# Optimization experiments

Measured on AMD Instinct MI355X. Metric: run time of the kernel, lower is better.

The kernel has to match this reference:

```python
import jax, jax.numpy as jnp
import numpy as np

B, D, S, L = 4, 512, 2048, 8921

def setup_inputs() -> dict:
    key = jax.random.key(0)
    ks = jax.random.split(key, 4)
    H = jax.random.normal(ks[0], (B, D, S), dtype=jnp.float32)
    # 1x1 conv weights collapse to [out, in] matrices (xavier-ish scale)
    Wk = jax.random.normal(ks[1], (D, D), dtype=jnp.float32) * (1.0 / np.sqrt(D))
    Wv = jax.random.normal(ks[2], (D, D), dtype=jnp.float32) * (1.0 / np.sqrt(D))
    bk = jnp.full((D,), 0.01, dtype=jnp.float32)
    bv = jnp.full((D,), 0.01, dtype=jnp.float32)
    Q = jax.random.normal(ks[3], (L, D), dtype=jnp.float32) * 0.02
    return {"H": H, "Wk": Wk, "bk": bk, "Wv": Wv, "bv": bv, "Q": Q}

def reference(H, Wk, bk, Wv, bv, Q):
    # K/V: 1x1 Conv1d over channels + bias, ELU, permute(0,2,1) -> [B,S,D]
    K = jax.nn.elu(jnp.einsum('od,bds->bso', Wk, H) + bk)
    V = jax.nn.elu(jnp.einsum('od,bds->bso', Wv, H) + bv)
    # TargetAttention: energy E = Q K^T -> [B,L,S], softmax over seq (scale=False)
    E = jnp.einsum('ld,bsd->bls', Q, K)
    A = jax.nn.softmax(E, axis=-1)
    C = jnp.einsum('bls,bsd->bld', A, V)  # [B, L, D]
    return (C, A)
```

## Files before the change

kernel.cpp:

```cpp
#include <hip/hip_runtime.h>
#include <math.h>

#define Bn 4
#define Dn 512
#define Sn 2048
#define Ln 8921
#define Lpad 8960

typedef short bf16x8 __attribute__((ext_vector_type(8)));
typedef float f32x4 __attribute__((ext_vector_type(4)));

__device__ __forceinline__ float elu1(float x) {
    return x > 0.f ? x : expm1f(x);
}

__device__ __forceinline__ unsigned f2bf(float f) {
    unsigned u = __float_as_uint(f);
    u += 0x7FFFu + ((u >> 16) & 1u);
    return u >> 16;
}
__device__ __forceinline__ unsigned pack2(float a, float b) {
    return f2bf(a) | (f2bf(b) << 16);
}
__device__ __forceinline__ unsigned pack_bf_trunc(float lo, float hi) {
    return __builtin_amdgcn_perm(__float_as_uint(hi), __float_as_uint(lo), 0x07060302u);
}
__device__ __forceinline__ void gld_lds16(const void* g, void* l) {
    __builtin_amdgcn_global_load_lds((const __attribute__((address_space(1))) int*)g,
                                     (__attribute__((address_space(3))) int*)l, 16, 0, 0);
}

__global__ __launch_bounds__(256) void h_transpose(const float* __restrict__ H,
                                                   short* __restrict__ Ht) {
    int b = blockIdx.z;
    int s0 = blockIdx.x * 64, d0 = blockIdx.y * 64;
    __shared__ float tile[64][65];
    int t = threadIdx.x;
    int r = t >> 4, c4 = (t & 15) * 4;
    const float* Hb = H + (size_t)b * Dn * Sn;
#pragma unroll
    for (int i = 0; i < 4; ++i) {
        float4 v = *(const float4*)(Hb + (size_t)(d0 + i * 16 + r) * Sn + s0 + c4);
        *(float4*)&tile[i * 16 + r][c4] = v;
    }
    __syncthreads();
#pragma unroll
    for (int i = 0; i < 4; ++i) {
        int srow = i * 16 + r;
        float v0 = tile[c4 + 0][srow], v1 = tile[c4 + 1][srow];
        float v2 = tile[c4 + 2][srow], v3 = tile[c4 + 3][srow];
        uint2 o = make_uint2(pack2(v0, v1), pack2(v2, v3));
        *(uint2*)(Ht + ((size_t)b * Sn + s0 + srow) * Dn + d0 + c4) = o;
    }
}

__global__ __launch_bounds__(256) void f32_to_bf16(const float* __restrict__ src,
                                                   short* __restrict__ dst, int n8) {
    int id = blockIdx.x * 256 + threadIdx.x;
    if (id >= n8) return;
    const float* s = src + (size_t)id * 8;
    float4 a = *(const float4*)s;
    float4 b = *(const float4*)(s + 4);
    uint4 o = {pack2(a.x, a.y), pack2(a.z, a.w), pack2(b.x, b.y), pack2(b.z, b.w)};
    *(uint4*)(dst + (size_t)id * 8) = o;
}

__global__ __launch_bounds__(256) void q_to_bf16(const float* __restrict__ Q,
                                                 short* __restrict__ Qb) {
    int id = blockIdx.x * 256 + threadIdx.x;
    int row = id >> 6, c = (id & 63) * 8;
    uint4 o = {0, 0, 0, 0};
    if (row < Ln) {
        const float* src = Q + (size_t)row * Dn + c;
        float4 a = *(const float4*)src;
        float4 b = *(const float4*)(src + 4);
        o.x = pack2(a.x, a.y); o.y = pack2(a.z, a.w);
        o.z = pack2(b.x, b.y); o.w = pack2(b.z, b.w);
    }
    *(uint4*)(Qb + (size_t)id * 8) = o;
}

template <int OUT_BF16, int EPI>
__global__ __launch_bounds__(256) void gemm_nt(const short* __restrict__ A,
                                               const short* __restrict__ B,
                                               const float* __restrict__ bias,
                                               void* __restrict__ Out,
                                               int K, int lda, int ldb, int ldo,
                                               int mmax,
                                               long bA, long bB, long bO) {
    const int b  = blockIdx.z;
    const int n0 = blockIdx.x * 128;
    const int m0 = blockIdx.y * 128;
    __shared__ short lA[128 * 32];
    __shared__ short lB[128 * 32];
    const int t = threadIdx.x;
    const int lane = t & 63, w = t >> 6;
    const int wm = (w & 1) * 64, wn = (w >> 1) * 64;
    const int quad = lane >> 4, l15 = lane & 15;
    f32x4 acc[4][4] = {};
    const short* Ab = A + (size_t)bA * b + (size_t)m0 * lda;
    const short* Bb = B + (size_t)bB * b + (size_t)n0 * ldb;
    const int sr = t >> 2, ss = (t & 3) * 8;

    for (int k0 = 0; k0 < K; k0 += 32) {
        gld_lds16(Ab + (size_t)sr * lda + k0 + ss,        lA + t * 8);
        gld_lds16(Ab + (size_t)(sr + 64) * lda + k0 + ss, lA + 2048 + t * 8);
        gld_lds16(Bb + (size_t)sr * ldb + k0 + ss,        lB + t * 8);
        gld_lds16(Bb + (size_t)(sr + 64) * ldb + k0 + ss, lB + 2048 + t * 8);
        __syncthreads();
        bf16x8 af[4], bfr[4];
#pragma unroll
        for (int i = 0; i < 4; ++i)
            af[i] = *(const bf16x8*)&lA[(wm + i * 16 + l15) * 32 + quad * 8];
#pragma unroll
        for (int j = 0; j < 4; ++j)
            bfr[j] = *(const bf16x8*)&lB[(wn + j * 16 + l15) * 32 + quad * 8];
#pragma unroll
        for (int i = 0; i < 4; ++i)
#pragma unroll
            for (int j = 0; j < 4; ++j)
                acc[i][j] = __builtin_amdgcn_mfma_f32_16x16x32_bf16(af[i], bfr[j], acc[i][j], 0, 0, 0);
        __syncthreads();
    }

#pragma unroll
    for (int i = 0; i < 4; ++i) {
        int mb = m0 + wm + i * 16 + quad * 4;
#pragma unroll
        for (int r = 0; r < 4; ++r) {
            int m = mb + r;
            if (m < mmax) {
                float bm = (EPI == 2) ? bias[m] : 0.f;
#pragma unroll
                for (int j = 0; j < 4; ++j) {
                    int col = n0 + wn + j * 16 + l15;
                    float v = acc[i][j][r];
                    if (EPI == 1) v = elu1(v + bias[col]);
                    if (EPI == 2) v = elu1(v + bm);
                    if (OUT_BF16)
                        ((short*)Out)[(size_t)bO * b + (size_t)m * ldo + col] = (short)f2bf(v);
                    else
                        ((float*)Out)[(size_t)bO * b + (size_t)m * ldo + col] = v;
                }
            }
        }
    }
}

template <int OUT_BF16, int BN>
__global__ __launch_bounds__(512, 2) void gemm_ntp(const short* __restrict__ A,
                                                   const short* __restrict__ B,
                                                   void* __restrict__ Out,
                                                   int K, int lda, int ldb, int ldo,
                                                   int mmax,
                                                   long bA, long bB, long bO) {
    constexpr int NWN   = BN / 64;
    constexpr int WSPAN = 32 * NWN;
    constexpr int WMF   = 2 * NWN;
    constexpr int BCH   = BN * 4;
    constexpr int SLOT  = 8192 + BN * 32;
    constexpr int TPB   = 2 + BN / 128;
    __shared__ short lds[4 * SLOT];

    int GX = gridDim.x, GY = gridDim.y;
    int nwg = GX * GY * gridDim.z;
    int lin = blockIdx.x + GX * (blockIdx.y + GY * blockIdx.z);
    int wid = lin;
    if ((nwg & 7) == 0) wid = (lin & 7) * (nwg >> 3) + (lin >> 3);
    int bx = wid % GX; wid /= GX;
    int by = wid % GY;
    int bz = wid / GY;

    const int b  = bz;
    const int n0 = bx * BN;
    const int m0 = by * 256;
    const int t = threadIdx.x;
    const int lane = t & 63, w = t >> 6;
    const int wn = w % NWN, wm = w / NWN;
    const int quad = lane >> 4, l15 = lane & 15;
    const int xr = (l15 >> 1) & 3;

    const short* Ab = A + (size_t)bA * b + (size_t)m0 * lda;
    const short* Bb = B + (size_t)bB * b + (size_t)n0 * ldb;

    const short* srcA[2]; int dstA[2];
#pragma unroll
    for (int i = 0; i < 2; ++i) {
        int p = i * 512 + t;
        int g = p ^ ((p >> 3) & 3);
        srcA[i] = Ab + (size_t)(g >> 2) * lda + (g & 3) * 8;
        dstA[i] = p * 8;
    }
    const short* srcB[2]; int dstB[2];
#pragma unroll
    for (int i = 0; i < BCH / 512; ++i) {
        int p = i * 512 + t;
        int g = p ^ ((p >> 3) & 3);
        srcB[i] = Bb + (size_t)(g >> 2) * ldb + (g & 3) * 8;
        dstB[i] = 8192 + p * 8;
    }

    int offA[WMF], offB[4];
#pragma unroll
    for (int m = 0; m < WMF; ++m) {
        int c = (wm * WSPAN + m * 16 + l15) * 4 + quad;
        offA[m] = (c ^ xr) * 8;
    }
#pragma unroll
    for (int j = 0; j < 4; ++j) {
        int c = (wn * 64 + j * 16 + l15) * 4 + quad;
        offB[j] = 8192 + (c ^ xr) * 8;
    }

    f32x4 acc[WMF][4] = {};
    const int NK = K >> 5;

    auto STAGE_A = [&](int kt) {
        const int slot = (kt & 3) * SLOT;
        const int ko = kt * 32;
        gld_lds16(srcA[0] + ko, &lds[slot + dstA[0]]);
        gld_lds16(srcA[1] + ko, &lds[slot + dstA[1]]);
    };
    auto STAGE_B = [&](int kt) {
        const int slot = (kt & 3) * SLOT;
        const int ko = kt * 32;
        gld_lds16(srcB[0] + ko, &lds[slot + dstB[0]]);
        if constexpr (BN == 256) gld_lds16(srcB[1] + ko, &lds[slot + dstB[1]]);
    };

    STAGE_A(0); STAGE_B(0);
    STAGE_A(1); STAGE_B(1);
    STAGE_A(2); STAGE_B(2);

    for (int k = 0; k < NK; ++k) {
        asm volatile("s_waitcnt lgkmcnt(0)" ::: "memory");
        if constexpr (TPB == 4) {
            if (k < NK - 2)       asm volatile("s_waitcnt vmcnt(8)" ::: "memory");
            else if (k == NK - 2) asm volatile("s_waitcnt vmcnt(4)" ::: "memory");
            else                  asm volatile("s_waitcnt vmcnt(0)" ::: "memory");
        } else {
            if (k < NK - 2)       asm volatile("s_waitcnt vmcnt(6)" ::: "memory");
            else if (k == NK - 2) asm volatile("s_waitcnt vmcnt(3)" ::: "memory");
            else                  asm volatile("s_waitcnt vmcnt(0)" ::: "memory");
        }
        __builtin_amdgcn_s_barrier();
        asm volatile("" ::: "memory");
        const short* sl = &lds[(k & 3) * SLOT];

        bf16x8 af[WMF], bfv[4];
#pragma unroll
        for (int j = 0; j < 4; ++j) bfv[j] = *(const bf16x8*)(sl + offB[j]);
#pragma unroll
        for (int m = 0; m < WMF / 2; ++m) af[m] = *(const bf16x8*)(sl + offA[m]);
        if (k + 3 < NK) STAGE_A(k + 3);
        asm volatile("s_waitcnt lgkmcnt(0)" ::: "memory");
        __builtin_amdgcn_s_barrier();
        __builtin_amdgcn_s_setprio(1);
#pragma unroll
        for (int m = 0; m < WMF / 2; ++m)
#pragma unroll
            for (int j = 0; j < 4; ++j)
                acc[m][j] = __builtin_amdgcn_mfma_f32_16x16x32_bf16(af[m], bfv[j], acc[m][j], 0, 0, 0);
        __builtin_amdgcn_s_setprio(0);
        __builtin_amdgcn_s_barrier();

#pragma unroll
        for (int m = WMF / 2; m < WMF; ++m) af[m] = *(const bf16x8*)(sl + offA[m]);
        if (k + 3 < NK) STAGE_B(k + 3);
        asm volatile("s_waitcnt lgkmcnt(0)" ::: "memory");
        __builtin_amdgcn_s_barrier();
        __builtin_amdgcn_s_setprio(1);
#pragma unroll
        for (int m = WMF / 2; m < WMF; ++m)
#pragma unroll
            for (int j = 0; j < 4; ++j)
                acc[m][j] = __builtin_amdgcn_mfma_f32_16x16x32_bf16(af[m], bfv[j], acc[m][j], 0, 0, 0);
        __builtin_amdgcn_s_setprio(0);
    }

#pragma unroll
    for (int m = 0; m < WMF; ++m) {
        int mb = m0 + wm * WSPAN + m * 16 + quad * 4;
#pragma unroll
        for (int r = 0; r < 4; ++r) {
            int mm = mb + r;
            if (mm < mmax) {
#pragma unroll
                for (int j = 0; j < 4; ++j) {
                    int col = n0 + wn * 64 + j * 16 + l15;
                    float v = acc[m][j][r];
                    if (OUT_BF16)
                        ((short*)Out)[(size_t)bO * b + (size_t)mm * ldo + col] = (short)f2bf(v);
                    else
                        ((float*)Out)[(size_t)bO * b + (size_t)mm * ldo + col] = v;
                }
            }
        }
    }
}

__global__ __launch_bounds__(256) void softmax_bf16(short* __restrict__ EA,
                                                    float* __restrict__ Aout) {
    int row = blockIdx.x;
    int b = row / Ln, l = row - b * Ln;
    short* pe = EA + ((size_t)b * Lpad + l) * Sn;
    float* pa = Aout + (size_t)row * Sn;
    int t = threadIdx.x;
    uint4 raw = *(const uint4*)(pe + t * 8);
    unsigned pw[4] = {raw.x, raw.y, raw.z, raw.w};
    float v[8];
#pragma unroll
    for (int q = 0; q < 4; ++q) {
        v[2 * q]     = __uint_as_float(pw[q] << 16);
        v[2 * q + 1] = __uint_as_float(pw[q] & 0xFFFF0000u);
    }
    float m = v[0];
#pragma unroll
    for (int i = 1; i < 8; ++i) m = fmaxf(m, v[i]);
#pragma unroll
    for (int off = 32; off >= 1; off >>= 1) m = fmaxf(m, __shfl_xor(m, off));
    __shared__ float sm[4], ssum[4];
    int lane = t & 63, wv = t >> 6;
    if (lane == 0) sm[wv] = m;
    __syncthreads();
    m = fmaxf(fmaxf(sm[0], sm[1]), fmaxf(sm[2], sm[3]));
    float s = 0.f;
#pragma unroll
    for (int i = 0; i < 8; ++i) {
        v[i] = expf(v[i] - m);
        s += v[i];
    }
#pragma unroll
    for (int off = 32; off >= 1; off >>= 1) s += __shfl_xor(s, off);
    if (lane == 0) ssum[wv] = s;
    __syncthreads();
    s = ssum[0] + ssum[1] + ssum[2] + ssum[3];
    float inv = 1.f / s;
#pragma unroll
    for (int i = 0; i < 8; ++i) v[i] *= inv;
    float4 o0 = {v[0], v[1], v[2], v[3]};
    float4 o1 = {v[4], v[5], v[6], v[7]};
    *(float4*)(pa + t * 8)     = o0;
    *(float4*)(pa + t * 8 + 4) = o1;
    uint4 ob = {pack2(v[0], v[1]), pack2(v[2], v[3]), pack2(v[4], v[5]), pack2(v[6], v[7])};
    *(uint4*)(pe + t * 8) = ob;
}

__global__ __launch_bounds__(256) void softmax_f32(float* __restrict__ E) {
    size_t row = blockIdx.x;
    float* p = E + row * (size_t)Sn;
    int t = threadIdx.x;
    float4 u0 = *(const float4*)(p + t * 8);
    float4 u1 = *(const float4*)(p + t * 8 + 4);
    float v[8] = {u0.x, u0.y, u0.z, u0.w, u1.x, u1.y, u1.z, u1.w};
    float m = v[0];
#pragma unroll
    for (int i = 1; i < 8; ++i) m = fmaxf(m, v[i]);
#pragma unroll
    for (int off = 32; off >= 1; off >>= 1) m = fmaxf(m, __shfl_xor(m, off));
    __shared__ float sm[4], ssum[4];
    int lane = t & 63, wv = t >> 6;
    if (lane == 0) sm[wv] = m;
    __syncthreads();
    m = fmaxf(fmaxf(sm[0], sm[1]), fmaxf(sm[2], sm[3]));
    float s = 0.f;
#pragma unroll
    for (int i = 0; i < 8; ++i) {
        v[i] = expf(v[i] - m);
        s += v[i];
    }
#pragma unroll
    for (int off = 32; off >= 1; off >>= 1) s += __shfl_xor(s, off);
    if (lane == 0) ssum[wv] = s;
    __syncthreads();
    s = ssum[0] + ssum[1] + ssum[2] + ssum[3];
    float inv = 1.f / s;
#pragma unroll
    for (int i = 0; i < 8; ++i) v[i] *= inv;
    float4 o0 = {v[0], v[1], v[2], v[3]};
    float4 o1 = {v[4], v[5], v[6], v[7]};
    *(float4*)(p + t * 8)     = o0;
    *(float4*)(p + t * 8 + 4) = o1;
}

__global__ __launch_bounds__(256) void c_mfma_f32(const float* __restrict__ A,
                                                  const short* __restrict__ Vt,
                                                  float* __restrict__ C) {
    const int b  = blockIdx.z;
    const int n0 = blockIdx.x * 128;
    const int m0 = blockIdx.y * 128;
    __shared__ short lA[128 * 32];
    __shared__ short lB[128 * 32];
    const int t = threadIdx.x;
    const int lane = t & 63, w = t >> 6;
    const int wm = (w & 1) * 64, wn = (w >> 1) * 64;
    const int quad = lane >> 4, l15 = lane & 15;
    f32x4 acc[4][4] = {};
    const float* Ab = A + (size_t)b * Ln * Sn;
    const short* Bb = Vt + (size_t)b * Dn * Sn + (size_t)n0 * Sn;
    const int ar = t >> 1, ah = (t & 1) * 16;
    const int br = t >> 2, bs = (t & 3) * 8;
    const int am = m0 + ar;
    const bool arow_ok = (am < Ln);
    const float* asrc0 = Ab + (size_t)am * Sn + ah;

    for (int s0 = 0; s0 < Sn; s0 += 32) {
        gld_lds16(Bb + (size_t)br * Sn + s0 + bs,        lB + t * 8);
        gld_lds16(Bb + (size_t)(br + 64) * Sn + s0 + bs, lB + 2048 + t * 8);
        unsigned p[8] = {0, 0, 0, 0, 0, 0, 0, 0};
        if (arow_ok) {
            const float* src = asrc0 + s0;
            float4 f0 = *(const float4*)(src);
            float4 f1 = *(const float4*)(src + 4);
            float4 f2 = *(const float4*)(src + 8);
            float4 f3 = *(const float4*)(src + 12);
            p[0] = pack_bf_trunc(f0.x, f0.y); p[1] = pack_bf_trunc(f0.z, f0.w);
            p[2] = pack_bf_trunc(f1.x, f1.y); p[3] = pack_bf_trunc(f1.z, f1.w);
            p[4] = pack_bf_trunc(f2.x, f2.y); p[5] = pack_bf_trunc(f2.z, f2.w);
            p[6] = pack_bf_trunc(f3.x, f3.y); p[7] = pack_bf_trunc(f3.z, f3.w);
        }
        *(uint4*)&lA[ar * 32 + ah]     = *(uint4*)&p[0];
        *(uint4*)&lA[ar * 32 + ah + 8] = *(uint4*)&p[4];
        __syncthreads();
        bf16x8 af[4], bfr[4];
#pragma unroll
        for (int i = 0; i < 4; ++i)
            af[i] = *(const bf16x8*)&lA[(wm + i * 16 + l15) * 32 + quad * 8];
#pragma unroll
        for (int j = 0; j < 4; ++j)
            bfr[j] = *(const bf16x8*)&lB[(wn + j * 16 + l15) * 32 + quad * 8];
#pragma unroll
        for (int i = 0; i < 4; ++i)
#pragma unroll
            for (int j = 0; j < 4; ++j)
                acc[i][j] = __builtin_amdgcn_mfma_f32_16x16x32_bf16(af[i], bfr[j], acc[i][j], 0, 0, 0);
        __syncthreads();
    }

#pragma unroll
    for (int i = 0; i < 4; ++i) {
        int mb = m0 + wm + i * 16 + quad * 4;
#pragma unroll
        for (int r = 0; r < 4; ++r) {
            int m = mb + r;
            if (m < Ln) {
                float* dst = C + (size_t)b * Ln * Dn + (size_t)m * Dn + n0 + wn;
#pragma unroll
                for (int j = 0; j < 4; ++j) dst[j * 16 + l15] = acc[i][j][r];
            }
        }
    }
}

extern "C" void kernel_launch(void* const* d_in, const int* in_sizes, int n_in,
                              void* d_out, int out_size, void* d_ws, size_t ws_size,
                              hipStream_t stream) {
    const float* H  = (const float*)d_in[0];
    const float* Wk = (const float*)d_in[1];
    const float* bk = (const float*)d_in[2];
    const float* Wv = (const float*)d_in[3];
    const float* bv = (const float*)d_in[4];
    const float* Q  = (const float*)d_in[5];

    float* out  = (float*)d_out;
    float* Cout = out;
    float* Aout = out + (size_t)Bn * Ln * Dn;

    short* Vt  = (short*)d_ws;
    short* Kb  = Vt + (size_t)Bn * Dn * Sn;
    short* Qb  = Kb + (size_t)Bn * Sn * Dn;
    short* EAb = Qb + (size_t)Lpad * Dn;
    short* Ht  = EAb;
    short* Wkb = Ht + (size_t)Bn * Sn * Dn;
    short* Wvb = Wkb + (size_t)Dn * Dn;

    size_t need_primary =
        2 * ((size_t)Bn * Dn * Sn + (size_t)Bn * Sn * Dn + (size_t)Lpad * Dn +
             (size_t)Bn * Lpad * Sn);
    bool big = ws_size >= need_primary;

    h_transpose<<<dim3(Sn / 64, Dn / 64, Bn), 256, 0, stream>>>(H, Ht);
    f32_to_bf16<<<(Dn * Dn / 8 + 255) / 256, 256, 0, stream>>>(Wk, Wkb, Dn * Dn / 8);
    f32_to_bf16<<<(Dn * Dn / 8 + 255) / 256, 256, 0, stream>>>(Wv, Wvb, Dn * Dn / 8);
    q_to_bf16<<<(Lpad * 64) / 256, 256, 0, stream>>>(Q, Qb);

    gemm_nt<1, 1><<<dim3(Dn / 128, Sn / 128, Bn), 256, 0, stream>>>(
        Ht, Wkb, bk, Kb, Dn, Dn, Dn, Dn, Sn,
        (long)Sn * Dn, 0L, (long)Sn * Dn);

    gemm_nt<1, 2><<<dim3(Sn / 128, Dn / 128, Bn), 256, 0, stream>>>(
        Wvb, Ht, bv, Vt, Dn, Dn, Dn, Sn, Dn,
        0L, (long)Sn * Dn, (long)Dn * Sn);

    if (big) {
        gemm_ntp<1, 256><<<dim3(Sn / 256, Lpad / 256, Bn), 512, 0, stream>>>(
            Qb, Kb, EAb, Dn, Dn, Dn, Sn, Lpad,
            0L, (long)Sn * Dn, (long)Lpad * Sn);
        softmax_bf16<<<Bn * Ln, 256, 0, stream>>>(EAb, Aout);
        gemm_ntp<0, 128><<<dim3(Dn / 128, Lpad / 256, Bn), 512, 0, stream>>>(
            EAb, Vt, Cout, Sn, Sn, Sn, Dn, Ln,
            (long)Lpad * Sn, (long)Dn * Sn, (long)Ln * Dn);
    } else {
        gemm_nt<0, 0><<<dim3(Sn / 128, Lpad / 128, Bn), 256, 0, stream>>>(
            Qb, Kb, nullptr, Aout, Dn, Dn, Dn, Sn, Ln,
            0L, (long)Sn * Dn, (long)Ln * Sn);
        softmax_f32<<<Bn * Ln, 256, 0, stream>>>(Aout);
        c_mfma_f32<<<dim3(Dn / 128, Lpad / 128, Bn), 256, 0, stream>>>(Aout, Vt, Cout);
    }
}
```

Measured before the change: 724.6 us.

## Fuse softmax normalization into the A·V GEMM using per-row stats

```diff
diff --git a/kernel.cpp b/kernel.cpp
--- a/kernel.cpp
+++ b/kernel.cpp
@@ -299,11 +299,13 @@
     }
 }
 
-__global__ __launch_bounds__(256) void softmax_bf16(short* __restrict__ EA,
-                                                    float* __restrict__ Aout) {
+__global__ __launch_bounds__(256) void softmax_stats(const short* __restrict__ EA,
+                                                     float* __restrict__ Aout,
+                                                     float2* __restrict__ Stat) {
+    const float c1 = 1.44269504088896340736f;
     int row = blockIdx.x;
     int b = row / Ln, l = row - b * Ln;
-    short* pe = EA + ((size_t)b * Lpad + l) * Sn;
+    const short* pe = EA + ((size_t)b * Lpad + l) * Sn;
     float* pa = Aout + (size_t)row * Sn;
     int t = threadIdx.x;
     uint4 raw = *(const uint4*)(pe + t * 8);
@@ -324,10 +326,11 @@
     if (lane == 0) sm[wv] = m;
     __syncthreads();
     m = fmaxf(fmaxf(sm[0], sm[1]), fmaxf(sm[2], sm[3]));
+    float ebase = -m * c1;
     float s = 0.f;
 #pragma unroll
     for (int i = 0; i < 8; ++i) {
-        v[i] = expf(v[i] - m);
+        v[i] = exp2f(fmaf(v[i], c1, ebase));
         s += v[i];
     }
 #pragma unroll
@@ -342,8 +345,147 @@
     float4 o1 = {v[4], v[5], v[6], v[7]};
     *(float4*)(pa + t * 8)     = o0;
     *(float4*)(pa + t * 8 + 4) = o1;
-    uint4 ob = {pack2(v[0], v[1]), pack2(v[2], v[3]), pack2(v[4], v[5]), pack2(v[6], v[7])};
-    *(uint4*)(pe + t * 8) = ob;
+    if (t == 0) Stat[(size_t)b * Lpad + l] = make_float2(m, inv);
+}
+
+__global__ __launch_bounds__(512, 2) void c_fused(const short* __restrict__ E,
+                                                  const short* __restrict__ Vt,
+                                                  const float2* __restrict__ Stat,
+                                                  float* __restrict__ C) {
+    constexpr int NK   = Sn / 32;
+    constexpr int ASZ  = 256 * 32;
+    constexpr int SLOT = ASZ + 128 * 32;
+    __shared__ short lds[2 * SLOT];
+    const float c1 = 1.44269504088896340736f;
+
+    int GX = gridDim.x, GY = gridDim.y;
+    int nwg = GX * GY * gridDim.z;
+    int lin = blockIdx.x + GX * (blockIdx.y + GY * blockIdx.z);
+    int wid = lin;
+    if ((nwg & 7) == 0) wid = (lin & 7) * (nwg >> 3) + (lin >> 3);
+    int bx = wid % GX; wid /= GX;
+    int by = wid % GY;
+    int bz = wid / GY;
+    const int b = bz, n0 = bx * 128, m0 = by * 256;
+
+    const int t = threadIdx.x, lane = t & 63, w = t >> 6;
+    const int wn = w & 1, wm = w >> 1;
+    const int quad = lane >> 4, l15 = lane & 15;
+    const int xr = (l15 >> 1) & 3;
+
+    const short* Eb = E + ((size_t)b * Lpad + m0) * Sn;
+    const short* Bb = Vt + (size_t)b * Dn * Sn + (size_t)n0 * Sn;
+
+    const int bg = t ^ ((t >> 3) & 3);
+    const short* srcB = Bb + (size_t)(bg >> 2) * Sn + (bg & 3) * 8;
+    const int dstB = ASZ + t * 8;
+
+    const int er = t >> 1, eh = (t & 1) * 16;
+    const short* srcE = Eb + (size_t)er * Sn + eh;
+    float2 st = Stat[(size_t)b * Lpad + m0 + er];
+    const float ebase = -st.x * c1;
+    const float inv = st.y;
+    const int ac0 = er * 4 + (t & 1) * 2;
+    const int wp0 = (ac0 ^ ((ac0 >> 3) & 3)) * 8;
+    const int wp1 = ((ac0 + 1) ^ (((ac0 + 1) >> 3) & 3)) * 8;
+
+    int offA[4], offB[4];
+#pragma unroll
+    for (int m = 0; m < 4; ++m) {
+        int c = (wm * 64 + m * 16 + l15) * 4 + quad;
+        offA[m] = (c ^ xr) * 8;
+    }
+#pragma unroll
+    for (int j = 0; j < 4; ++j) {
+        int c = (wn * 64 + j * 16 + l15) * 4 + quad;
+        offB[j] = ASZ + (c ^ xr) * 8;
+    }
+
+    f32x4 acc[4][4] = {};
+
+    auto ELOAD = [&](int kt, uint4& lo, uint4& hi) {
+        const short* p0 = srcE + kt * 32;
+        asm volatile("global_load_dwordx4 %0, %1, off" : "=&v"(lo) : "v"(p0));
+        asm volatile("global_load_dwordx4 %0, %1, off" : "=&v"(hi) : "v"(p0 + 8));
+    };
+    auto BSTAGE = [&](int kt) {
+        gld_lds16(srcB + kt * 32, &lds[(kt & 1) * SLOT + dstB]);
+    };
+    auto EPROC = [&](int kt, const uint4& lo, const uint4& hi) {
+        unsigned pw[8] = {lo.x, lo.y, lo.z, lo.w, hi.x, hi.y, hi.z, hi.w};
+        unsigned pk[8];
+#pragma unroll
+        for (int q = 0; q < 8; ++q) {
+            float a = __uint_as_float(pw[q] << 16);
+            float c = __uint_as_float(pw[q] & 0xFFFF0000u);
+            float pa = exp2f(fmaf(a, c1, ebase)) * inv;
+            float pc = exp2f(fmaf(c, c1, ebase)) * inv;
+            pk[q] = pack2(pa, pc);
+        }
+        short* sl = &lds[(kt & 1) * SLOT];
+        *(uint4*)&sl[wp0] = make_uint4(pk[0], pk[1], pk[2], pk[3]);
+        *(uint4*)&sl[wp1] = make_uint4(pk[4], pk[5], pk[6], pk[7]);
+    };
+
+    uint4 eA0, eA1, eB0, eB1;
+    BSTAGE(0);
+    ELOAD(0, eA0, eA1);
+    ELOAD(1, eB0, eB1);
+    asm volatile("s_waitcnt vmcnt(2)" ::: "memory");
+    __builtin_amdgcn_sched_barrier(0);
+    EPROC(0, eA0, eA1);
+    asm volatile("s_waitcnt lgkmcnt(0)" ::: "memory");
+    __builtin_amdgcn_s_barrier();
+
+    auto ITER = [&](int k, const uint4& epLo, const uint4& epHi,
+                    uint4& elLo, uint4& elHi) {
+        const bool haveN  = (k + 1 < NK);
+        const bool haveNN = (k + 2 < NK);
+        if (haveN)  BSTAGE(k + 1);
+        if (haveNN) ELOAD(k + 2, elLo, elHi);
+        const short* sl = &lds[(k & 1) * SLOT];
+        bf16x8 af[4], bfv[4];
+#pragma unroll
+        for (int m = 0; m < 4; ++m) af[m] = *(const bf16x8*)(sl + offA[m]);
+#pragma unroll
+        for (int j = 0; j < 4; ++j) bfv[j] = *(const bf16x8*)(sl + offB[j]);
+        __builtin_amdgcn_s_setprio(1);
+#pragma unroll
+        for (int m = 0; m < 4; ++m)
+#pragma unroll
+            for (int j = 0; j < 4; ++j)
+                acc[m][j] = __builtin_amdgcn_mfma_f32_16x16x32_bf16(af[m], bfv[j], acc[m][j], 0, 0, 0);
+        __builtin_amdgcn_s_setprio(0);
+        if (haveN) {
+            if (haveNN) asm volatile("s_waitcnt vmcnt(3)" ::: "memory");
+            else        asm volatile("s_waitcnt vmcnt(1)" ::: "memory");
+            __builtin_amdgcn_sched_barrier(0);
+            EPROC(k + 1, epLo, epHi);
+            if (haveNN) asm volatile("s_waitcnt vmcnt(2)" ::: "memory");
+            else        asm volatile("s_waitcnt vmcnt(0)" ::: "memory");
+            asm volatile("s_waitcnt lgkmcnt(0)" ::: "memory");
+            __builtin_amdgcn_s_barrier();
+        }
+    };
+
+    for (int kk = 0; kk < NK; kk += 2) {
+        ITER(kk,     eB0, eB1, eA0, eA1);
+        ITER(kk + 1, eA0, eA1, eB0, eB1);
+    }
+
+#pragma unroll
+    for (int m = 0; m < 4; ++m) {
+        int mb = m0 + wm * 64 + m * 16 + quad * 4;
+#pragma unroll
+        for (int r = 0; r < 4; ++r) {
+            int mm = mb + r;
+            if (mm < Ln) {
+                float* dst = C + (size_t)b * Ln * Dn + (size_t)mm * Dn + n0 + wn * 64;
+#pragma unroll
+                for (int j = 0; j < 4; ++j) dst[j * 16 + l15] = acc[m][j][r];
+            }
+        }
+    }
 }
 
 __global__ __launch_bounds__(256) void softmax_f32(float* __restrict__ E) {
@@ -470,13 +612,14 @@
     short* Kb  = Vt + (size_t)Bn * Dn * Sn;
     short* Qb  = Kb + (size_t)Bn * Sn * Dn;
     short* EAb = Qb + (size_t)Lpad * Dn;
+    float2* Stat = (float2*)(EAb + (size_t)Bn * Lpad * Sn);
     short* Ht  = EAb;
     short* Wkb = Ht + (size_t)Bn * Sn * Dn;
     short* Wvb = Wkb + (size_t)Dn * Dn;
 
     size_t need_primary =
         2 * ((size_t)Bn * Dn * Sn + (size_t)Bn * Sn * Dn + (size_t)Lpad * Dn +
-             (size_t)Bn * Lpad * Sn);
+             (size_t)Bn * Lpad * Sn) + 8 * (size_t)Bn * Lpad;
     bool big = ws_size >= need_primary;
 
     h_transpose<<<dim3(Sn / 64, Dn / 64, Bn), 256, 0, stream>>>(H, Ht);
@@ -496,10 +639,9 @@
         gemm_ntp<1, 256><<<dim3(Sn / 256, Lpad / 256, Bn), 512, 0, stream>>>(
             Qb, Kb, EAb, Dn, Dn, Dn, Sn, Lpad,
             0L, (long)Sn * Dn, (long)Lpad * Sn);
-        softmax_bf16<<<Bn * Ln, 256, 0, stream>>>(EAb, Aout);
-        gemm_ntp<0, 128><<<dim3(Dn / 128, Lpad / 256, Bn), 512, 0, stream>>>(
-            EAb, Vt, Cout, Sn, Sn, Sn, Dn, Ln,
-            (long)Lpad * Sn, (long)Dn * Sn, (long)Ln * Dn);
+        softmax_stats<<<Bn * Ln, 256, 0, stream>>>(EAb, Aout, Stat);
+        c_fused<<<dim3(Dn / 128, Lpad / 256, Bn), 512, 0, stream>>>(
+            EAb, Vt, Stat, Cout);
     } else {
         gemm_nt<0, 0><<<dim3(Sn / 128, Lpad / 128, Bn), 256, 0, stream>>>(
             Qb, Kb, nullptr, Aout, Dn, Dn, Dn, Sn, Ln,
```

New measurement: 783.1 us. +8.1%, slower.
